# Performance work log

Measured on AMD Instinct MI355X. Metric: run time of the kernel, lower is better.

The kernel has to match this reference:

```python
import jax, jax.numpy as jnp
import numpy as np

MIN_CONN, MAX_CONN = 1, 16
RATIO = 0.25
EPS_NORM = 1e-12   # F.normalize eps
GN_EPS = 1e-5
NUM_GROUPS = 32    # largest divisor of C=128 that is <= 32


def setup_inputs() -> dict:
    key = jax.random.key(0)
    ks = jax.random.split(key, 3)
    B, C, H, W = 2, 128, 48, 48
    x = jax.random.normal(ks[0], (B, C, H, W), dtype=jnp.float32)
    gamma = jnp.ones((C,), jnp.float32)
    beta = jnp.zeros((C,), jnp.float32)
    w1 = jax.random.normal(ks[1], (2 * C, C), jnp.float32) * 0.02
    b1 = jnp.zeros((2 * C,), jnp.float32)
    w2 = jax.random.normal(ks[2], (C, 2 * C), jnp.float32) * 0.02
    b2 = jnp.zeros((C,), jnp.float32)
    return {"x": x, "gamma": gamma, "beta": beta, "w1": w1, "b1": b1, "w2": w2, "b2": b2}


def _connection_counts(x):
    B, C, H, W = x.shape
    xd = jax.image.resize(x, (B, C, H // 2, W // 2), method='bilinear', antialias=False)
    xdu = jax.image.resize(xd, (B, C, H, W), method='bilinear', antialias=False)
    df = jnp.abs(x - xdu).sum(axis=1, keepdims=True)  # [B,1,H,W]
    dmin = df.reshape(B, -1).min(axis=1).reshape(B, 1, 1, 1)
    dmax = df.reshape(B, -1).max(axis=1).reshape(B, 1, 1, 1)
    dn = (df - dmin) / (dmax - dmin + 1e-8)
    return MIN_CONN + jnp.round(dn * (MAX_CONN - MIN_CONN))  # [B,1,H,W] float


def _ipg_forward(x, gamma, beta, w1, b1, w2, b2):
    B, C, H, W = x.shape
    cc = _connection_counts(x)

    win = max(3, int(min(H, W) * RATIO))
    if win % 2 == 0:
        win += 1
    K2 = win * win
    pad = win // 2

    xp = jnp.pad(x, ((0, 0), (0, 0), (pad, pad), (pad, pad)), mode='reflect')
    # unfold -> [B, C, K2, H, W] with torch ordering (row-major over (i,j))
    patches = jnp.stack([xp[:, :, i:i + H, j:j + W]
                         for i in range(win) for j in range(win)], axis=2)
    patches = patches.reshape(B, C, K2, H * W).transpose(0, 3, 1, 2)  # [B,P,C,K2]

    x_flat = x.reshape(B, C, H * W).transpose(0, 2, 1)  # [B,P,C]
    x_norm = x_flat / jnp.maximum(jnp.linalg.norm(x_flat, axis=-1, keepdims=True), EPS_NORM)
    pnorm = jnp.maximum(jnp.sqrt((patches ** 2).sum(axis=2)), EPS_NORM)  # [B,P,K2]
    sim = jnp.einsum('bpck,bpc->bpk', patches, x_norm) / pnorm  # [B,P,K2]

    # variable-k topk as a rank mask: rank(sim descending) < k, then exp-softmax over selected
    k = jnp.minimum(cc.reshape(B, H * W), float(K2))  # [B,P]
    ranks = jnp.argsort(jnp.argsort(-sim, axis=-1), axis=-1)  # [B,P,K2]
    mask = ranks < k[..., None]
    w = jnp.exp(sim) * mask
    w = w / w.sum(axis=-1, keepdims=True)
    out = jnp.einsum('bpck,bpk->bpc', patches, w)  # [B,P,C]
    out = out.transpose(0, 2, 1).reshape(B, C, H, W)

    # GroupNorm(32, C)
    xg = x.reshape(B, NUM_GROUPS, C // NUM_GROUPS, H, W)
    mu = xg.mean(axis=(2, 3, 4), keepdims=True)
    var = xg.var(axis=(2, 3, 4), keepdims=True)
    xn = ((xg - mu) / jnp.sqrt(var + GN_EPS)).reshape(B, C, H, W)
    norm_x = xn * gamma[None, :, None, None] + beta[None, :, None, None]

    enhanced = out + norm_x
    # 1x1 conv FFN
    h = jnp.einsum('oc,bchw->bohw', w1, enhanced) + b1[None, :, None, None]
    h = jax.nn.relu(h)
    ffn = jnp.einsum('oc,bchw->bohw', w2, h) + b2[None, :, None, None]
    return enhanced + ffn


def reference(x, gamma, beta, w1, b1, w2, b2):
    return _ipg_forward(x, gamma, beta, w1, b1, w2, b2)
```

## Files before the change

kernel.cpp:

```cpp
#include <hip/hip_runtime.h>

constexpr int CH = 128;
constexpr int WW = 48;
constexpr int PP = 2304;
constexpr int NPIX = 4608;
constexpr int K2 = 169;

constexpr size_t OFF_XT  = 0;
constexpr size_t OFF_RN  = OFF_XT + (size_t)NPIX * CH;
constexpr size_t OFF_DF  = OFF_RN + NPIX;
constexpr size_t OFF_GNP = OFF_DF + NPIX;
constexpr size_t OFF_MMP = OFF_GNP + 288 * 16;
constexpr size_t OFF_W1T = OFF_MMP + 144;
constexpr size_t OFF_W2T = OFF_W1T + 32768;
constexpr size_t WS_FLOATS = OFF_W2T + 32768;

__device__ __forceinline__ int refl(int t) {
    return t < 0 ? -t : (t > 47 ? 94 - t : t);
}

__global__ __launch_bounds__(256) void kA(const float* __restrict__ x,
                                          const float* __restrict__ w1,
                                          const float* __restrict__ w2,
                                          float* __restrict__ xt,
                                          float* __restrict__ gnp,
                                          float* __restrict__ w1t,
                                          float* __restrict__ w2t,
                                          float* __restrict__ df,
                                          float* __restrict__ rn,
                                          float* __restrict__ mmp) {
    __shared__ union { float t[32][65]; float red[4][64][2]; } sm;
    const int tid = threadIdx.x;
    const int bid = blockIdx.x;
    if (bid < 288) {
        const int tile = bid >> 2, q = bid & 3;
        const int p0 = tile * 64;
        const int b = p0 / PP, pb = p0 % PP;
        const int pl = tid & 63, cb = tid >> 6;
        const float* xb = x + (size_t)b * CH * PP + (size_t)(q * 32) * PP + pb;
#pragma unroll
        for (int r = 0; r < 8; r++) {
            int c = r * 4 + cb;
            sm.t[c][pl] = xb[(size_t)c * PP + pl];
        }
        __syncthreads();
        {
            const int c4 = tid & 7, pq = tid >> 3;
#pragma unroll
            for (int r = 0; r < 2; r++) {
                int px = r * 32 + pq;
                float4 v = make_float4(sm.t[c4 * 4][px], sm.t[c4 * 4 + 1][px],
                                       sm.t[c4 * 4 + 2][px], sm.t[c4 * 4 + 3][px]);
                ((float4*)(xt + (size_t)(p0 + px) * CH + q * 32))[c4] = v;
            }
        }
        {
            const int j = tid >> 5, part = tid & 31;
            float s = 0.f, sq = 0.f;
#pragma unroll
            for (int pi = 0; pi < 2; pi++) {
                int px = part * 2 + pi;
#pragma unroll
                for (int i = 0; i < 4; i++) {
                    float v = sm.t[j * 4 + i][px];
                    s += v; sq += v * v;
                }
            }
#pragma unroll
            for (int m = 16; m; m >>= 1) { s += __shfl_xor(s, m); sq += __shfl_xor(sq, m); }
            if (part == 0) { gnp[bid * 16 + j * 2] = s; gnp[bid * 16 + j * 2 + 1] = sq; }
        }
    } else if (bid < 360) {
        const int strip = bid - 288;
        const int p0 = strip * 64;
        const int b = p0 / PP;
        const int wv = tid >> 6, lane = tid & 63;
        const int p = (p0 % PP) + lane;
        const int h = p / WW, w = p % WW;
        float py = 0.5f * h - 0.25f; int y0 = (int)floorf(py); float fy = py - (float)y0;
        float px_ = 0.5f * w - 0.25f; int x0 = (int)floorf(px_); float fx = px_ - (float)x0;
        int y0c = max(y0, 0), y1c = min(y0 + 1, 23);
        int x0c = max(x0, 0), x1c = min(x0 + 1, 23);
        float q00 = 0.25f * (1.f - fy) * (1.f - fx), q01 = 0.25f * (1.f - fy) * fx;
        float q10 = 0.25f * fy * (1.f - fx),        q11 = 0.25f * fy * fx;
        int r0 = (2 * y0c) * WW, r1 = (2 * y0c + 1) * WW;
        int r2 = (2 * y1c) * WW, r3 = (2 * y1c + 1) * WW;
        int ca = 2 * x0c, cb2 = 2 * x1c;
        const float* xc = x + (size_t)b * CH * PP + (size_t)(wv * 32) * PP;
        float ds = 0.f, ss = 0.f;
        for (int c = 0; c < 32; c++) {
            const float* xp = xc + (size_t)c * PP;
            float xv = xp[p];
            float s00 = xp[r0 + ca] + xp[r0 + ca + 1] + xp[r1 + ca] + xp[r1 + ca + 1];
            float s01 = xp[r0 + cb2] + xp[r0 + cb2 + 1] + xp[r1 + cb2] + xp[r1 + cb2 + 1];
            float s10 = xp[r2 + ca] + xp[r2 + ca + 1] + xp[r3 + ca] + xp[r3 + ca + 1];
            float s11 = xp[r2 + cb2] + xp[r2 + cb2 + 1] + xp[r3 + cb2] + xp[r3 + cb2 + 1];
            float up = q00 * s00 + q01 * s01 + q10 * s10 + q11 * s11;
            ds += fabsf(xv - up);
            ss += xv * xv;
        }
        sm.red[wv][lane][0] = ds; sm.red[wv][lane][1] = ss;
        __syncthreads();
        if (wv == 0) {
            float dst = sm.red[0][lane][0] + sm.red[1][lane][0] +
                        sm.red[2][lane][0] + sm.red[3][lane][0];
            float sst = sm.red[0][lane][1] + sm.red[1][lane][1] +
                        sm.red[2][lane][1] + sm.red[3][lane][1];
            df[p0 + lane] = dst;
            rn[p0 + lane] = 1.f / fmaxf(sqrtf(sst), 1e-12f);
            float mn = dst, mx = dst;
#pragma unroll
            for (int m = 32; m; m >>= 1) {
                mn = fminf(mn, __shfl_xor(mn, m));
                mx = fmaxf(mx, __shfl_xor(mx, m));
            }
            if (lane == 0) { mmp[strip * 2] = mn; mmp[strip * 2 + 1] = mx; }
        }
    } else {
        int idx = (bid - 360) * 256 + tid;
        if (idx < 32768) {
            int o = idx >> 7, c = idx & 127;
            w1t[(size_t)((c >> 2) * 256 + o) * 4 + (c & 3)] = w1[idx];
        } else {
            int i2 = idx - 32768;
            int c = i2 >> 8, oo = i2 & 255;
            w2t[(size_t)((oo >> 2) * 128 + c) * 4 + (oo & 3)] = w2[i2];
        }
    }
}

__global__ __launch_bounds__(256, 2) void kB(const float* __restrict__ xt,
                                             const float* __restrict__ rn,
                                             const float* __restrict__ df,
                                             const float* __restrict__ mmp,
                                             const float* __restrict__ gnp,
                                             const float* __restrict__ gamma,
                                             const float* __restrict__ beta,
                                             const float* __restrict__ w1t,
                                             const float* __restrict__ w2t,
                                             const float* __restrict__ b1f,
                                             const float* __restrict__ b2f,
                                             float* __restrict__ out) {
    __shared__ union {
        struct { float sims[4][176]; int kl[4][16]; float wl[4][16]; } a;
        struct { float elds[4][128]; float hlds[4][256]; } f;
    } sm;
    __shared__ float gnbl[32][2];
    __shared__ float mml[2];
    const int tid = threadIdx.x, wv = tid >> 6, lane = tid & 63;
    const int base = blockIdx.x * 4;
    const int b = base / PP;

    if (tid < 32) {
        const int g = tid, q = g >> 3, j = g & 7;
        float s = 0.f, sq = 0.f;
#pragma unroll 4
        for (int t2 = 0; t2 < 36; t2++) {
            int u = (b * 36 + t2) * 4 + q;
            s += gnp[u * 16 + j * 2];
            sq += gnp[u * 16 + j * 2 + 1];
        }
        float mu = s / 9216.f;
        float var = sq / 9216.f - mu * mu;
        gnbl[g][0] = mu;
        gnbl[g][1] = 1.f / sqrtf(var + 1e-5f);
    } else if (tid >= 64 && tid < 128) {
        int i = tid - 64;
        float mn = 1e30f, mx = -1e30f;
        if (i < 36) { mn = mmp[(b * 36 + i) * 2]; mx = mmp[(b * 36 + i) * 2 + 1]; }
#pragma unroll
        for (int m = 32; m; m >>= 1) {
            mn = fminf(mn, __shfl_xor(mn, m));
            mx = fmaxf(mx, __shfl_xor(mx, m));
        }
        if (i == 0) { mml[0] = mn; mml[1] = mx; }
    }
    __syncthreads();
    const float dmin = mml[0], dmax = mml[1];

    const int pix = base + wv;
    const int p = pix % PP;
    const int h = p / WW, w = p % WW;
    const int bb = b * PP;
    const int g16 = lane >> 2, cl2 = lane & 3;

    float4 ctr[8];
    const float4* cp = (const float4*)(xt + (size_t)pix * CH);
#pragma unroll
    for (int c = 0; c < 8; c++) ctr[c] = cp[c * 4 + cl2];
    const float rnp = rn[pix];

    if (lane < 16) { sm.a.kl[wv][lane] = 0; sm.a.wl[wv][lane] = -1e30f; }

#pragma unroll 2
    for (int kb = 0; kb < 176; kb += 16) {
        const int k = kb + g16;
        const int krow = k / 13, kcol = k - krow * 13;
        const int yy = refl(h + krow - 6), xx = refl(w + kcol - 6);
        const int p2 = bb + yy * WW + xx;
        const float4* rp = (const float4*)(xt + (size_t)p2 * CH);
        float dot = 0.f;
#pragma unroll
        for (int c = 0; c < 8; c++) {
            float4 v = rp[c * 4 + cl2];
            dot += v.x * ctr[c].x + v.y * ctr[c].y + v.z * ctr[c].z + v.w * ctr[c].w;
        }
        dot += __shfl_xor(dot, 1);
        dot += __shfl_xor(dot, 2);
        float s = dot * rnp * rn[p2];
        if (cl2 == 0 && k < K2) sm.a.sims[wv][k] = s;
    }

    float s0 = sm.a.sims[wv][lane];
    float s1 = sm.a.sims[wv][64 + lane];
    float s2 = (128 + lane < K2) ? sm.a.sims[wv][128 + lane] : -1e30f;
    const float dn = (df[pix] - dmin) / (dmax - dmin + 1e-8f);
    const int cc = 1 + (int)rintf(dn * 15.f);

    for (int i = 0; i < cc; ++i) {
        float gm = fmaxf(fmaxf(s0, s1), s2);
#pragma unroll
        for (int sft = 1; sft <= 32; sft <<= 1) gm = fmaxf(gm, __shfl_xor(gm, sft));
        unsigned long long m0 = __ballot(s0 == gm);
        unsigned long long m1 = __ballot(s1 == gm);
        unsigned long long m2 = __ballot(s2 == gm);
        int kw = m0 ? (__ffsll(m0) - 1)
               : m1 ? (64 + __ffsll(m1) - 1)
                    : (128 + __ffsll(m2) - 1);
        bool me = (lane == (kw & 63));
        s0 = (me && kw < 64) ? -1e30f : s0;
        s1 = (me && kw >= 64 && kw < 128) ? -1e30f : s1;
        s2 = (me && kw >= 128) ? -1e30f : s2;
        if (lane == 0) { sm.a.kl[wv][i] = kw; sm.a.wl[wv][i] = gm; }
    }

    float wsum = 0.f, ax = 0.f, ay = 0.f;
#pragma unroll
    for (int i = 0; i < 16; ++i) {
        const int kw = sm.a.kl[wv][i];
        const float sv = sm.a.wl[wv][i];
        const float wt = expf(sv);
        const int krow = kw / 13, kcol = kw - krow * 13;
        const int p2 = bb + refl(h + krow - 6) * WW + refl(w + kcol - 6);
        float2 v = ((const float2*)(xt + (size_t)p2 * CH))[lane];
        wsum += wt; ax += wt * v.x; ay += wt * v.y;
    }
    const float invw = 1.f / wsum;

    float2 xv = ((const float2*)(xt + (size_t)pix * CH))[lane];
    const int c0 = lane * 2, grp = lane >> 1;
    const float mu = gnbl[grp][0], rstd = gnbl[grp][1];
    float e0 = ax * invw + (xv.x - mu) * rstd * gamma[c0] + beta[c0];
    float e1 = ay * invw + (xv.y - mu) * rstd * gamma[c0 + 1] + beta[c0 + 1];

    __syncthreads();
    ((float2*)sm.f.elds[wv])[lane] = make_float2(e0, e1);
    __syncthreads();

    {
        float acc4[4] = {0.f, 0.f, 0.f, 0.f};
        const float4* wp = ((const float4*)w1t) + tid;
        for (int c4 = 0; c4 < 32; c4++) {
            float4 wv4 = wp[c4 * 256];
#pragma unroll
            for (int px = 0; px < 4; px++) {
                float4 ev = *(const float4*)&sm.f.elds[px][c4 * 4];
                acc4[px] += wv4.x * ev.x + wv4.y * ev.y + wv4.z * ev.z + wv4.w * ev.w;
            }
        }
        float bv = b1f[tid];
#pragma unroll
        for (int px = 0; px < 4; px++)
            sm.f.hlds[px][tid] = fmaxf(acc4[px] + bv, 0.f);
    }
    __syncthreads();
    {
        const int c = tid & 127, hf = tid >> 7;
        const int px0 = hf * 2;
        float acc2[2] = {0.f, 0.f};
        const float4* wp2 = ((const float4*)w2t) + c;
        for (int o4 = 0; o4 < 64; o4++) {
            float4 wv4 = wp2[o4 * 128];
#pragma unroll
            for (int j = 0; j < 2; j++) {
                float4 hv = *(const float4*)&sm.f.hlds[px0 + j][o4 * 4];
                acc2[j] += wv4.x * hv.x + wv4.y * hv.y + wv4.z * hv.z + wv4.w * hv.w;
            }
        }
        float bv = b2f[c];
        float2 o2;
        o2.x = sm.f.elds[px0 + 0][c] + acc2[0] + bv;
        o2.y = sm.f.elds[px0 + 1][c] + acc2[1] + bv;
        *(float2*)(out + ((size_t)(b * CH + c)) * PP + (base % PP) + px0) = o2;
    }
}

extern "C" void kernel_launch(void* const* d_in, const int* in_sizes, int n_in,
                              void* d_out, int out_size, void* d_ws, size_t ws_size,
                              hipStream_t stream) {
    (void)in_sizes; (void)n_in; (void)out_size;
    if (ws_size < WS_FLOATS * sizeof(float)) return;

    const float* x     = (const float*)d_in[0];
    const float* gamma = (const float*)d_in[1];
    const float* beta  = (const float*)d_in[2];
    const float* w1    = (const float*)d_in[3];
    const float* b1    = (const float*)d_in[4];
    const float* w2    = (const float*)d_in[5];
    const float* b2    = (const float*)d_in[6];
    float* ws = (float*)d_ws;
    float* xt  = ws + OFF_XT;
    float* rn  = ws + OFF_RN;
    float* df  = ws + OFF_DF;
    float* gnp = ws + OFF_GNP;
    float* mmp = ws + OFF_MMP;
    float* w1t = ws + OFF_W1T;
    float* w2t = ws + OFF_W2T;
    float* out = (float*)d_out;

    hipLaunchKernelGGL(kA, dim3(616),  dim3(256), 0, stream,
                       x, w1, w2, xt, gnp, w1t, w2t, df, rn, mmp);
    hipLaunchKernelGGL(kB, dim3(1152), dim3(256), 0, stream,
                       xt, rn, df, mmp, gnp, gamma, beta, w1t, w2t, b1, b2, out);
}
```

Baseline: 70.07 us.

## Split similarity computation into a separate kernel writing sims to workspace

Moves the 169-neighbour cosine-similarity dot products out of the fused kernel into a new kernel that uses two waves per pixel (each covering half the window) and 8 lanes per neighbour, writing results to a global workspace buffer. The main kernel then reads similarities from global memory instead of computing them. This is meant to raise parallelism and occupancy for the gather-heavy similarity phase and shrink the register footprint of the fused kernel. In exchange it adds a kernel launch and a round trip of about 3 MB through global memory.

```diff
diff --git a/kernel.cpp b/kernel.cpp
--- a/kernel.cpp
+++ b/kernel.cpp
@@ -6,13 +6,14 @@
 constexpr int NPIX = 4608;
 constexpr int K2 = 169;
 
-constexpr size_t OFF_XT  = 0;
-constexpr size_t OFF_RN  = OFF_XT + (size_t)NPIX * CH;
-constexpr size_t OFF_DF  = OFF_RN + NPIX;
-constexpr size_t OFF_GNP = OFF_DF + NPIX;
-constexpr size_t OFF_MMP = OFF_GNP + 288 * 16;
-constexpr size_t OFF_W1T = OFF_MMP + 144;
-constexpr size_t OFF_W2T = OFF_W1T + 32768;
+constexpr size_t OFF_XT   = 0;
+constexpr size_t OFF_SIMS = OFF_XT + (size_t)NPIX * CH;
+constexpr size_t OFF_RN   = OFF_SIMS + (size_t)NPIX * 176;
+constexpr size_t OFF_DF   = OFF_RN + NPIX;
+constexpr size_t OFF_GNP  = OFF_DF + NPIX;
+constexpr size_t OFF_MMP  = OFF_GNP + 288 * 16;
+constexpr size_t OFF_W1T  = OFF_MMP + 144;
+constexpr size_t OFF_W2T  = OFF_W1T + 32768;
 constexpr size_t WS_FLOATS = OFF_W2T + 32768;
 
 __device__ __forceinline__ int refl(int t) {
@@ -129,7 +130,47 @@
     }
 }
 
+__global__ __launch_bounds__(256) void kS(const float* __restrict__ xt,
+                                          const float* __restrict__ rn,
+                                          float* __restrict__ simsw) {
+    const int tid = threadIdx.x, wv = tid >> 6, lane = tid & 63;
+    const int pix = blockIdx.x * 2 + (wv & 1);
+    const int half = wv >> 1;
+    const int p = pix % PP;
+    const int h = p / WW, w = p % WW;
+    const int bb = (pix / PP) * PP;
+    const int g8 = lane >> 3, cl = lane & 7;
+
+    float4 ctr[4];
+    const float4* cp = (const float4*)(xt + (size_t)pix * CH) + cl;
+#pragma unroll
+    for (int c = 0; c < 4; c++) ctr[c] = cp[c * 8];
+    const float rnp = rn[pix];
+
+    const int kb0 = half * 88;
+#pragma unroll 2
+    for (int it = 0; it < 11; ++it) {
+        const int k = kb0 + it * 8 + g8;
+        const int krow = k / 13, kcol = k - krow * 13;
+        const int yy = refl(h + krow - 6), xx = refl(w + kcol - 6);
+        const int p2 = bb + yy * WW + xx;
+        const float4* rp = (const float4*)(xt + (size_t)p2 * CH) + cl;
+        float dot = 0.f;
+#pragma unroll
+        for (int c = 0; c < 4; c++) {
+            float4 v = rp[c * 8];
+            dot += v.x * ctr[c].x + v.y * ctr[c].y + v.z * ctr[c].z + v.w * ctr[c].w;
+        }
+        dot += __shfl_xor(dot, 1);
+        dot += __shfl_xor(dot, 2);
+        dot += __shfl_xor(dot, 4);
+        if (cl == 0 && k < K2)
+            simsw[(size_t)pix * 176 + k] = dot * rnp * rn[p2];
+    }
+}
+
 __global__ __launch_bounds__(256, 2) void kB(const float* __restrict__ xt,
+                                             const float* __restrict__ simsw,
                                              const float* __restrict__ rn,
                                              const float* __restrict__ df,
                                              const float* __restrict__ mmp,
@@ -142,7 +183,7 @@
                                              const float* __restrict__ b2f,
                                              float* __restrict__ out) {
     __shared__ union {
-        struct { float sims[4][176]; int kl[4][16]; float wl[4][16]; } a;
+        struct { int kl[4][16]; float wl[4][16]; } a;
         struct { float elds[4][128]; float hlds[4][256]; } f;
     } sm;
     __shared__ float gnbl[32][2];
@@ -175,45 +216,21 @@
         }
         if (i == 0) { mml[0] = mn; mml[1] = mx; }
     }
-    __syncthreads();
-    const float dmin = mml[0], dmax = mml[1];
 
     const int pix = base + wv;
     const int p = pix % PP;
     const int h = p / WW, w = p % WW;
     const int bb = b * PP;
-    const int g16 = lane >> 2, cl2 = lane & 3;
-
-    float4 ctr[8];
-    const float4* cp = (const float4*)(xt + (size_t)pix * CH);
-#pragma unroll
-    for (int c = 0; c < 8; c++) ctr[c] = cp[c * 4 + cl2];
-    const float rnp = rn[pix];
+
+    const float* srow = simsw + (size_t)pix * 176;
+    float s0 = srow[lane];
+    float s1 = srow[64 + lane];
+    float s2 = (128 + lane < K2) ? srow[128 + lane] : -1e30f;
 
     if (lane < 16) { sm.a.kl[wv][lane] = 0; sm.a.wl[wv][lane] = -1e30f; }
-
-#pragma unroll 2
-    for (int kb = 0; kb < 176; kb += 16) {
-        const int k = kb + g16;
-        const int krow = k / 13, kcol = k - krow * 13;
-        const int yy = refl(h + krow - 6), xx = refl(w + kcol - 6);
-        const int p2 = bb + yy * WW + xx;
-        const float4* rp = (const float4*)(xt + (size_t)p2 * CH);
-        float dot = 0.f;
-#pragma unroll
-        for (int c = 0; c < 8; c++) {
-            float4 v = rp[c * 4 + cl2];
-            dot += v.x * ctr[c].x + v.y * ctr[c].y + v.z * ctr[c].z + v.w * ctr[c].w;
-        }
-        dot += __shfl_xor(dot, 1);
-        dot += __shfl_xor(dot, 2);
-        float s = dot * rnp * rn[p2];
-        if (cl2 == 0 && k < K2) sm.a.sims[wv][k] = s;
-    }
-
-    float s0 = sm.a.sims[wv][lane];
-    float s1 = sm.a.sims[wv][64 + lane];
-    float s2 = (128 + lane < K2) ? sm.a.sims[wv][128 + lane] : -1e30f;
+    __syncthreads();
+
+    const float dmin = mml[0], dmax = mml[1];
     const float dn = (df[pix] - dmin) / (dmax - dmin + 1e-8f);
     const int cc = 1 + (int)rintf(dn * 15.f);
 
@@ -309,17 +326,19 @@
     const float* w2    = (const float*)d_in[5];
     const float* b2    = (const float*)d_in[6];
     float* ws = (float*)d_ws;
-    float* xt  = ws + OFF_XT;
-    float* rn  = ws + OFF_RN;
-    float* df  = ws + OFF_DF;
-    float* gnp = ws + OFF_GNP;
-    float* mmp = ws + OFF_MMP;
-    float* w1t = ws + OFF_W1T;
-    float* w2t = ws + OFF_W2T;
-    float* out = (float*)d_out;
+    float* xt    = ws + OFF_XT;
+    float* simsw = ws + OFF_SIMS;
+    float* rn    = ws + OFF_RN;
+    float* df    = ws + OFF_DF;
+    float* gnp   = ws + OFF_GNP;
+    float* mmp   = ws + OFF_MMP;
+    float* w1t   = ws + OFF_W1T;
+    float* w2t   = ws + OFF_W2T;
+    float* out   = (float*)d_out;
 
     hipLaunchKernelGGL(kA, dim3(616),  dim3(256), 0, stream,
                        x, w1, w2, xt, gnp, w1t, w2t, df, rn, mmp);
+    hipLaunchKernelGGL(kS, dim3(2304), dim3(256), 0, stream, xt, rn, simsw);
     hipLaunchKernelGGL(kB, dim3(1152), dim3(256), 0, stream,
-                       xt, rn, df, mmp, gnp, gamma, beta, w1t, w2t, b1, b2, out);
-}
+                       xt, simsw, rn, df, mmp, gnp, gamma, beta, w1t, w2t, b1, b2, out);
+}
```

Measured after the change: 70.15 us. No clear change (+0.1%).

## Use 8-lane neighbor groups with two neighbors per iteration and batch FFN weight loads

Applied to the files above, without the earlier changes.

The similarity loop now gives each neighbor 8 lanes instead of 4 and handles two neighbors per iteration, so each lane holds only 4 center float4s and issues 8 independent loads per iteration. This aims to raise memory-level parallelism and cut register pressure. The __syncthreads for the min/max stats moves below the center loads so that load latency overlaps the reduction, and the kl/wl init moves after the sims loop. Both FFN matvec loops now prefetch 8 weight float4s into registers before the FMAs, to hide global load latency at the cost of more registers.

```diff
diff --git a/kernel.cpp b/kernel.cpp
--- a/kernel.cpp
+++ b/kernel.cpp
@@ -175,45 +175,55 @@
         }
         if (i == 0) { mml[0] = mn; mml[1] = mx; }
     }
-    __syncthreads();
-    const float dmin = mml[0], dmax = mml[1];
 
     const int pix = base + wv;
     const int p = pix % PP;
     const int h = p / WW, w = p % WW;
     const int bb = b * PP;
-    const int g16 = lane >> 2, cl2 = lane & 3;
-
-    float4 ctr[8];
-    const float4* cp = (const float4*)(xt + (size_t)pix * CH);
-#pragma unroll
-    for (int c = 0; c < 8; c++) ctr[c] = cp[c * 4 + cl2];
+    const int g8 = lane >> 3, cl = lane & 7;
+
+    float4 ctr[4];
+    const float4* cp = (const float4*)(xt + (size_t)pix * CH) + cl;
+#pragma unroll
+    for (int c = 0; c < 4; c++) ctr[c] = cp[c * 8];
     const float rnp = rn[pix];
-
-    if (lane < 16) { sm.a.kl[wv][lane] = 0; sm.a.wl[wv][lane] = -1e30f; }
-
-#pragma unroll 2
+    __syncthreads();
+
     for (int kb = 0; kb < 176; kb += 16) {
-        const int k = kb + g16;
-        const int krow = k / 13, kcol = k - krow * 13;
-        const int yy = refl(h + krow - 6), xx = refl(w + kcol - 6);
-        const int p2 = bb + yy * WW + xx;
-        const float4* rp = (const float4*)(xt + (size_t)p2 * CH);
-        float dot = 0.f;
-#pragma unroll
-        for (int c = 0; c < 8; c++) {
-            float4 v = rp[c * 4 + cl2];
-            dot += v.x * ctr[c].x + v.y * ctr[c].y + v.z * ctr[c].z + v.w * ctr[c].w;
-        }
-        dot += __shfl_xor(dot, 1);
-        dot += __shfl_xor(dot, 2);
-        float s = dot * rnp * rn[p2];
-        if (cl2 == 0 && k < K2) sm.a.sims[wv][k] = s;
+        const int ka = kb + g8;
+        const int kc = kb + 8 + g8;
+        const int ra = ka / 13, ca_ = ka - ra * 13;
+        const int rc_ = kc / 13, cc_ = kc - rc_ * 13;
+        const int pa = bb + refl(h + ra - 6) * WW + refl(w + ca_ - 6);
+        const int pc = bb + refl(h + rc_ - 6) * WW + refl(w + cc_ - 6);
+        const float4* rpa = (const float4*)(xt + (size_t)pa * CH) + cl;
+        const float4* rpc = (const float4*)(xt + (size_t)pc * CH) + cl;
+        float4 va0 = rpa[0],  va1 = rpa[8],  va2 = rpa[16], va3 = rpa[24];
+        float4 vc0 = rpc[0],  vc1 = rpc[8],  vc2 = rpc[16], vc3 = rpc[24];
+        float rna = rn[pa], rnc2 = rn[pc];
+        float da = va0.x * ctr[0].x + va0.y * ctr[0].y + va0.z * ctr[0].z + va0.w * ctr[0].w
+                 + va1.x * ctr[1].x + va1.y * ctr[1].y + va1.z * ctr[1].z + va1.w * ctr[1].w
+                 + va2.x * ctr[2].x + va2.y * ctr[2].y + va2.z * ctr[2].z + va2.w * ctr[2].w
+                 + va3.x * ctr[3].x + va3.y * ctr[3].y + va3.z * ctr[3].z + va3.w * ctr[3].w;
+        float dc = vc0.x * ctr[0].x + vc0.y * ctr[0].y + vc0.z * ctr[0].z + vc0.w * ctr[0].w
+                 + vc1.x * ctr[1].x + vc1.y * ctr[1].y + vc1.z * ctr[1].z + vc1.w * ctr[1].w
+                 + vc2.x * ctr[2].x + vc2.y * ctr[2].y + vc2.z * ctr[2].z + vc2.w * ctr[2].w
+                 + vc3.x * ctr[3].x + vc3.y * ctr[3].y + vc3.z * ctr[3].z + vc3.w * ctr[3].w;
+        da += __shfl_xor(da, 1); dc += __shfl_xor(dc, 1);
+        da += __shfl_xor(da, 2); dc += __shfl_xor(dc, 2);
+        da += __shfl_xor(da, 4); dc += __shfl_xor(dc, 4);
+        if (cl == 0) {
+            sm.a.sims[wv][ka] = da * rnp * rna;
+            if (kc < K2) sm.a.sims[wv][kc] = dc * rnp * rnc2;
+        }
     }
 
     float s0 = sm.a.sims[wv][lane];
     float s1 = sm.a.sims[wv][64 + lane];
     float s2 = (128 + lane < K2) ? sm.a.sims[wv][128 + lane] : -1e30f;
+    if (lane < 16) { sm.a.kl[wv][lane] = 0; sm.a.wl[wv][lane] = -1e30f; }
+
+    const float dmin = mml[0], dmax = mml[1];
     const float dn = (df[pix] - dmin) / (dmax - dmin + 1e-8f);
     const int cc = 1 + (int)rintf(dn * 15.f);
 
@@ -260,12 +270,19 @@
     {
         float acc4[4] = {0.f, 0.f, 0.f, 0.f};
         const float4* wp = ((const float4*)w1t) + tid;
-        for (int c4 = 0; c4 < 32; c4++) {
-            float4 wv4 = wp[c4 * 256];
-#pragma unroll
-            for (int px = 0; px < 4; px++) {
-                float4 ev = *(const float4*)&sm.f.elds[px][c4 * 4];
-                acc4[px] += wv4.x * ev.x + wv4.y * ev.y + wv4.z * ev.z + wv4.w * ev.w;
+        for (int c8 = 0; c8 < 4; c8++) {
+            float4 wbuf[8];
+#pragma unroll
+            for (int j = 0; j < 8; j++) wbuf[j] = wp[(c8 * 8 + j) * 256];
+#pragma unroll
+            for (int j = 0; j < 8; j++) {
+                const int c4 = c8 * 8 + j;
+#pragma unroll
+                for (int px = 0; px < 4; px++) {
+                    float4 ev = *(const float4*)&sm.f.elds[px][c4 * 4];
+                    acc4[px] += wbuf[j].x * ev.x + wbuf[j].y * ev.y +
+                                wbuf[j].z * ev.z + wbuf[j].w * ev.w;
+                }
             }
         }
         float bv = b1f[tid];
@@ -279,12 +296,19 @@
         const int px0 = hf * 2;
         float acc2[2] = {0.f, 0.f};
         const float4* wp2 = ((const float4*)w2t) + c;
-        for (int o4 = 0; o4 < 64; o4++) {
-            float4 wv4 = wp2[o4 * 128];
-#pragma unroll
-            for (int j = 0; j < 2; j++) {
-                float4 hv = *(const float4*)&sm.f.hlds[px0 + j][o4 * 4];
-                acc2[j] += wv4.x * hv.x + wv4.y * hv.y + wv4.z * hv.z + wv4.w * hv.w;
+        for (int o8 = 0; o8 < 8; o8++) {
+            float4 wbuf[8];
+#pragma unroll
+            for (int j = 0; j < 8; j++) wbuf[j] = wp2[(o8 * 8 + j) * 128];
+#pragma unroll
+            for (int j = 0; j < 8; j++) {
+                const int o4 = o8 * 8 + j;
+#pragma unroll
+                for (int jj = 0; jj < 2; jj++) {
+                    float4 hv = *(const float4*)&sm.f.hlds[px0 + jj][o4 * 4];
+                    acc2[jj] += wbuf[j].x * hv.x + wbuf[j].y * hv.y +
+                                wbuf[j].z * hv.z + wbuf[j].w * hv.w;
+                }
             }
         }
         float bv = b2f[c];
```

Result: faster. 63.44 us (-9.5%).
